# Performance work log

Hardware: AMD Instinct MI355X
Metric: run time of the kernel (lower is better)

Reference implementation:

```python
import jax, jax.numpy as jnp
import numpy as np

E, T, I, O = 8, 8192, 2048, 4096  # experts, total_tokens, in_features, out_features


def setup_inputs() -> dict:
    key = jax.random.key(0)
    k1, k2, k3 = jax.random.split(key, 3)
    inputs = jax.random.normal(k1, (T, I), dtype=jnp.float32)
    # lecun_normal-style scale for the (E, I, O) kernel (fan_in = I)
    kernel = jax.random.normal(k2, (E, I, O), dtype=jnp.float32) * (1.0 / np.float32(np.sqrt(I)))
    # nonzero bias so the ragged bias-expansion path is exercised
    bias = jax.random.normal(k3, (E, O), dtype=jnp.float32) * 0.02
    # tokens are sorted by expert; equal groups summing exactly to T
    group_sizes = jnp.full((E,), T // E, dtype=jnp.int32)
    return {"inputs": inputs, "group_sizes": group_sizes, "kernel": kernel, "bias": bias}


def reference(inputs, group_sizes, kernel, bias):
    # Ragged grouped GEMM: row block g of `inputs` (size group_sizes[g]) is
    # multiplied by kernel[g] of shape (I, O). Matches _ragged_dot with
    # out_first=False: contraction dims ((1,), (1,)), rhs group dim 0.
    out = jax.lax.ragged_dot(inputs, kernel, group_sizes)  # (T, O)
    # Per-group bias add: bias[e] broadcast over that expert's token block.
    expert_ids = jnp.repeat(jnp.arange(E), group_sizes, total_repeat_length=T)
    return out + bias[expert_ids]
```

## Files before the change

### kernel.cpp

```cpp
#include <hip/hip_runtime.h>


typedef short bf16x8 __attribute__((ext_vector_type(8)));
typedef float f32x4 __attribute__((ext_vector_type(4)));
typedef unsigned short u16x8 __attribute__((ext_vector_type(8)));

constexpr int Ecnt = 8;
constexpr int Ttok = 8192;
constexpr int Ifeat = 2048;
constexpr int Ofeat = 4096;
constexpr int BM = 128, BN = 128, BK = 32;

__device__ __forceinline__ unsigned short f2bf(float f) {
  unsigned u = __float_as_uint(f);
  unsigned r = (u + 0x7FFFu + ((u >> 16) & 1u)) >> 16;
  return (unsigned short)r;
}

__global__ __launch_bounds__(256) void cvt_a(const float* __restrict__ src,
                                             unsigned short* __restrict__ dst) {
  size_t i = ((size_t)blockIdx.x * 256 + threadIdx.x) * 8;
  float4 f0 = *(const float4*)(src + i);
  float4 f1 = *(const float4*)(src + i + 4);
  u16x8 v;
  v[0] = f2bf(f0.x); v[1] = f2bf(f0.y); v[2] = f2bf(f0.z); v[3] = f2bf(f0.w);
  v[4] = f2bf(f1.x); v[5] = f2bf(f1.y); v[6] = f2bf(f1.z); v[7] = f2bf(f1.w);
  *(u16x8*)(dst + i) = v;
}

__global__ __launch_bounds__(256) void cvt_b(const float* __restrict__ src,
                                             unsigned short* __restrict__ dst) {
  __shared__ float tile[64][33];
  const int e = blockIdx.z;
  const int i0 = blockIdx.y * 64;
  const int o0 = blockIdx.x * 32;
  const int tid = threadIdx.x;
  const int tx = tid & 31, ty = tid >> 5;
  const float* s = src + ((size_t)e * Ifeat + i0) * Ofeat + o0;
#pragma unroll
  for (int r = 0; r < 8; ++r) {
    int i = r * 8 + ty;
    tile[i][tx] = s[(size_t)i * Ofeat + tx];
  }
  __syncthreads();
  const int ox = tid >> 3;
  const int ic = (tid & 7) * 8;
  unsigned short* d = dst + ((size_t)e * Ofeat + o0 + ox) * Ifeat + i0 + ic;
  u16x8 v;
#pragma unroll
  for (int j = 0; j < 8; ++j) v[j] = f2bf(tile[ic + j][ox]);
  *(u16x8*)d = v;
}

__device__ __forceinline__ void ld16(const unsigned short* g, unsigned short* l) {
  __builtin_amdgcn_global_load_lds(
      (const __attribute__((address_space(1))) unsigned int*)g,
      (__attribute__((address_space(3))) unsigned int*)l, 16, 0, 0);
}

__global__ __launch_bounds__(256) void moe_gemm(
    const unsigned short* __restrict__ A,
    const unsigned short* __restrict__ Bt,
    const int* __restrict__ gs,
    const float* __restrict__ bias,
    float* __restrict__ C) {
  __shared__ unsigned short lA[BM * BK];
  __shared__ unsigned short lB[BN * BK];

  const int tid = threadIdx.x;
  const int row0 = blockIdx.x * BM;
  const int col0 = blockIdx.y * BN;

  int e = 0;
  {
    int cum = 0;
#pragma unroll
    for (int g = 0; g < Ecnt; ++g) {
      int s = gs[g];
      if (row0 >= cum + s) { cum += s; e = g + 1; }
    }
  }

  const unsigned short* Ag = A + (size_t)row0 * Ifeat;
  const unsigned short* Bg = Bt + ((size_t)e * Ofeat + col0) * Ifeat;

  const int wave = tid >> 6, lane = tid & 63;
  const int wm = (wave >> 1) * 64, wn = (wave & 1) * 64;
  const int lrow = lane & 15;
  const int kb = (lane >> 4) * 8;

  const int c0 = tid, c1 = tid + 256;
  const unsigned short* a0 = Ag + (size_t)(c0 >> 2) * Ifeat + (c0 & 3) * 8;
  const unsigned short* a1 = Ag + (size_t)(c1 >> 2) * Ifeat + (c1 & 3) * 8;
  const unsigned short* b0 = Bg + (size_t)(c0 >> 2) * Ifeat + (c0 & 3) * 8;
  const unsigned short* b1 = Bg + (size_t)(c1 >> 2) * Ifeat + (c1 & 3) * 8;
  unsigned short* la0 = lA + c0 * 8;
  unsigned short* la1 = lA + c1 * 8;
  unsigned short* lb0 = lB + c0 * 8;
  unsigned short* lb1 = lB + c1 * 8;

  f32x4 acc[4][4];
#pragma unroll
  for (int i = 0; i < 4; ++i)
#pragma unroll
    for (int j = 0; j < 4; ++j) acc[i][j] = (f32x4){0.f, 0.f, 0.f, 0.f};

  for (int k0 = 0; k0 < Ifeat; k0 += BK) {
    ld16(a0 + k0, la0);
    ld16(a1 + k0, la1);
    ld16(b0 + k0, lb0);
    ld16(b1 + k0, lb1);
    __syncthreads();

    bf16x8 af[4], bf[4];
#pragma unroll
    for (int mt = 0; mt < 4; ++mt)
      af[mt] = *(const bf16x8*)(lA + (wm + mt * 16 + lrow) * BK + kb);
#pragma unroll
    for (int nt = 0; nt < 4; ++nt)
      bf[nt] = *(const bf16x8*)(lB + (wn + nt * 16 + lrow) * BK + kb);

#pragma unroll
    for (int mt = 0; mt < 4; ++mt)
#pragma unroll
      for (int nt = 0; nt < 4; ++nt)
        acc[mt][nt] = __builtin_amdgcn_mfma_f32_16x16x32_bf16(
            af[mt], bf[nt], acc[mt][nt], 0, 0, 0);

    __syncthreads();
  }

  const int r0 = (lane >> 4) * 4;
  const int cc = lane & 15;
  const float* be = bias + (size_t)e * Ofeat;
#pragma unroll
  for (int mt = 0; mt < 4; ++mt) {
    const int row = row0 + wm + mt * 16 + r0;
#pragma unroll
    for (int nt = 0; nt < 4; ++nt) {
      const int col = col0 + wn + nt * 16 + cc;
      const float b = be[col];
      float* Cp = C + (size_t)row * Ofeat + col;
#pragma unroll
      for (int r = 0; r < 4; ++r) Cp[(size_t)r * Ofeat] = acc[mt][nt][r] + b;
    }
  }
}

extern "C" void kernel_launch(void* const* d_in, const int* in_sizes, int n_in,
                              void* d_out, int out_size, void* d_ws, size_t ws_size,
                              hipStream_t stream) {
  const float* inputs = (const float*)d_in[0];
  const int* group_sizes = (const int*)d_in[1];
  const float* kern = (const float*)d_in[2];
  const float* bias = (const float*)d_in[3];
  float* out = (float*)d_out;

  unsigned short* Abf = (unsigned short*)d_ws;
  unsigned short* Bbf = Abf + (size_t)Ttok * Ifeat;

  cvt_a<<<(Ttok * (size_t)Ifeat) / (8 * 256), 256, 0, stream>>>(inputs, Abf);
  cvt_b<<<dim3(Ofeat / 32, Ifeat / 64, Ecnt), 256, 0, stream>>>(kern, Bbf);

  moe_gemm<<<dim3(Ttok / BM, Ofeat / BN), 256, 0, stream>>>(Abf, Bbf, group_sizes,
                                                            bias, out);
}
```

Measured before the change: 669.5 us.

## Remap GEMM blocks by expert group and widen weight transpose tiles

The GEMM grid becomes 1D. Each run of 256 consecutive blocks covers one 1024-row group, with its 8 row tiles adjacent and then stepping across column tiles, so tiles sharing an expert's weight columns run close together for better L2 reuse. The layout hardcodes 1024 rows per group, i.e. equal group sizes, although the expert lookup still reads group_sizes. The weight transpose/convert kernel now handles 128 output columns per block with float4 loads and a padded shared-memory tile, aiming for wider, fewer global transactions.

Measured after the change: 638.2 us. 1.05x faster.

```diff
diff --git a/kernel.cpp b/kernel.cpp
--- a/kernel.cpp
+++ b/kernel.cpp
@@ -30,26 +30,39 @@
 
 __global__ __launch_bounds__(256) void cvt_b(const float* __restrict__ src,
                                              unsigned short* __restrict__ dst) {
-  __shared__ float tile[64][33];
+  constexpr int LDST = 129;
+  __shared__ float tile[64 * LDST];
   const int e = blockIdx.z;
   const int i0 = blockIdx.y * 64;
-  const int o0 = blockIdx.x * 32;
+  const int o0 = blockIdx.x * 128;
   const int tid = threadIdx.x;
-  const int tx = tid & 31, ty = tid >> 5;
-  const float* s = src + ((size_t)e * Ifeat + i0) * Ofeat + o0;
+
+  {
+    const int tx = tid & 31, ty = tid >> 5;
+    const float* s = src + ((size_t)e * Ifeat + i0) * Ofeat + o0 + tx * 4;
 #pragma unroll
-  for (int r = 0; r < 8; ++r) {
-    int i = r * 8 + ty;
-    tile[i][tx] = s[(size_t)i * Ofeat + tx];
+    for (int r = 0; r < 8; ++r) {
+      int i = r * 8 + ty;
+      float4 f = *(const float4*)(s + (size_t)i * Ofeat);
+      float* l = tile + i * LDST + tx * 4;
+      l[0] = f.x; l[1] = f.y; l[2] = f.z; l[3] = f.w;
+    }
   }
   __syncthreads();
-  const int ox = tid >> 3;
-  const int ic = (tid & 7) * 8;
-  unsigned short* d = dst + ((size_t)e * Ofeat + o0 + ox) * Ifeat + i0 + ic;
-  u16x8 v;
+  {
+    const int ic = (tid & 7) * 8;
+    const int oc = tid >> 3;
 #pragma unroll
-  for (int j = 0; j < 8; ++j) v[j] = f2bf(tile[ic + j][ox]);
-  *(u16x8*)d = v;
+    for (int p = 0; p < 4; ++p) {
+      int o = p * 32 + oc;
+      u16x8 v;
+#pragma unroll
+      for (int j = 0; j < 8; ++j) v[j] = f2bf(tile[(ic + j) * LDST + o]);
+      unsigned short* d =
+          dst + ((size_t)e * Ofeat + o0 + o) * Ifeat + i0 + ic;
+      *(u16x8*)d = v;
+    }
+  }
 }
 
 __device__ __forceinline__ void ld16(const unsigned short* g, unsigned short* l) {
@@ -68,8 +81,12 @@
   __shared__ unsigned short lB[BN * BK];
 
   const int tid = threadIdx.x;
-  const int row0 = blockIdx.x * BM;
-  const int col0 = blockIdx.y * BN;
+  const int bid = blockIdx.x;
+  const int eg = bid >> 8;
+  const int rt = (bid & 255) & 7;
+  const int ct = (bid & 255) >> 3;
+  const int row0 = eg * 1024 + rt * BM;
+  const int col0 = ct * BN;
 
   int e = 0;
   {
@@ -160,8 +177,8 @@
   unsigned short* Bbf = Abf + (size_t)Ttok * Ifeat;
 
   cvt_a<<<(Ttok * (size_t)Ifeat) / (8 * 256), 256, 0, stream>>>(inputs, Abf);
-  cvt_b<<<dim3(Ofeat / 32, Ifeat / 64, Ecnt), 256, 0, stream>>>(kern, Bbf);
+  cvt_b<<<dim3(Ofeat / 128, Ifeat / 64, Ecnt), 256, 0, stream>>>(kern, Bbf);
 
-  moe_gemm<<<dim3(Ttok / BM, Ofeat / BN), 256, 0, stream>>>(Abf, Bbf, group_sizes,
-                                                            bias, out);
+  moe_gemm<<<Ttok / BM * (Ofeat / BN), 256, 0, stream>>>(Abf, Bbf, group_sizes,
+                                                         bias, out);
 }
```
